# Kernel tuning notes

Measured on AMD Instinct MI355X. Metric: run time of the kernel, lower is better.

Reference implementation:

```python
import jax, jax.numpy as jnp
import numpy as np

DIM = 128
N_CONV = 4
N_GRAPHS = 256
EPS = 1e-5


def _layernorm(h, g, b):
    m = jnp.mean(h, axis=-1, keepdims=True)
    v = jnp.mean((h - m) ** 2, axis=-1, keepdims=True)
    return g * (h - m) / jnp.sqrt(v + 1e-5) + b


def _gated_gcn(x, ei, e, Wsrc, bsrc, Wdst, bdst, We, be, nxg, nxb, neg, neb):
    # x: [N, D] node feats, ei: [2, E], e: [E, D] edge feats
    n = x.shape[0]
    i, j = ei[0], ei[1]
    sig = jax.nn.sigmoid(e)                                   # [E, D]
    e_sum = jax.ops.segment_sum(sig, i, num_segments=n)       # [N, D]
    e_gated = sig / (e_sum[i] + EPS)                          # [E, D]
    msg = e_gated * (x[j] @ Wdst + bdst)                      # [E, D]
    agg = jax.ops.segment_sum(msg, i, num_segments=n)         # [N, D]
    out = x @ Wsrc + bsrc + agg
    out = x + jax.nn.silu(_layernorm(out, nxg, nxb))
    z = jnp.concatenate([x[i], x[j], e], axis=-1)             # [E, 3D]
    e_new = e + jax.nn.silu(_layernorm(z @ We + be, neg, neb))
    return out, e_new


def setup_inputs() -> dict:
    key = jax.random.key(0)
    ks = iter(jax.random.split(key, 64))
    d = DIM

    def rn(shape, s=0.05):
        return (jax.random.normal(next(ks), shape, dtype=jnp.float32) * s)

    inp = {}
    inp["x"] = jax.random.normal(next(ks), (20000, 92), dtype=jnp.float32)
    inp["edge_attr"] = jax.random.normal(next(ks), (320000, 50), dtype=jnp.float32)
    inp["edge_attr_line"] = jax.random.normal(next(ks), (600000, 40), dtype=jnp.float32)
    inp["edge_index"] = jax.random.randint(next(ks), (2, 320000), 0, 20000, dtype=jnp.int64)
    inp["edge_index_line"] = jax.random.randint(next(ks), (2, 600000), 0, 320000, dtype=jnp.int64)
    inp["batch"] = jnp.sort(jax.random.randint(next(ks), (20000,), 0, N_GRAPHS, dtype=jnp.int64))

    inp["pre1_W"] = rn((92, d)); inp["pre1_b"] = jnp.zeros((d,), jnp.float32)
    inp["pre2_W"] = rn((50, d)); inp["pre2_b"] = jnp.zeros((d,), jnp.float32)
    inp["pre3_W"] = rn((40, d)); inp["pre3_b"] = jnp.zeros((d,), jnp.float32)

    for pfx in ("line", "atom"):
        inp[pfx + "_Wsrc"] = rn((N_CONV, d, d)); inp[pfx + "_bsrc"] = jnp.zeros((N_CONV, d), jnp.float32)
        inp[pfx + "_Wdst"] = rn((N_CONV, d, d)); inp[pfx + "_bdst"] = jnp.zeros((N_CONV, d), jnp.float32)
        inp[pfx + "_We"] = rn((N_CONV, 3 * d, d)); inp[pfx + "_be"] = jnp.zeros((N_CONV, d), jnp.float32)
        inp[pfx + "_nxg"] = jnp.ones((N_CONV, d), jnp.float32); inp[pfx + "_nxb"] = jnp.zeros((N_CONV, d), jnp.float32)
        inp[pfx + "_neg"] = jnp.ones((N_CONV, d), jnp.float32); inp[pfx + "_neb"] = jnp.zeros((N_CONV, d), jnp.float32)

    inp["bn_g"] = jnp.ones((d,), jnp.float32); inp["bn_b"] = jnp.zeros((d,), jnp.float32)
    inp["post_W"] = rn((d, d)); inp["post_b"] = jnp.zeros((d,), jnp.float32)
    inp["out_W"] = rn((d, 1)); inp["out_b"] = jnp.zeros((1,), jnp.float32)
    return inp


def reference(x, edge_attr, edge_attr_line,
              pre1_W, pre1_b, pre2_W, pre2_b, pre3_W, pre3_b,
              line_Wsrc, line_bsrc, line_Wdst, line_bdst, line_We, line_be,
              line_nxg, line_nxb, line_neg, line_neb,
              atom_Wsrc, atom_bsrc, atom_Wdst, atom_bdst, atom_We, atom_be,
              atom_nxg, atom_nxb, atom_neg, atom_neb,
              bn_g, bn_b, post_W, post_b, out_W, out_b,
              edge_index, edge_index_line, batch):
    act = jax.nn.silu
    # pre-FC (single layer each)
    h_node = act(x @ pre1_W + pre1_b)              # [N, D]
    h_edge = act(edge_attr @ pre2_W + pre2_b)      # [E, D]
    h_line = act(edge_attr_line @ pre3_W + pre3_b) # [E_line, D]

    for l in range(N_CONV):
        # line graph conv: nodes = atom edges, edges = line-graph edges
        h_edge, h_line = _gated_gcn(h_edge, edge_index_line, h_line,
                                    line_Wsrc[l], line_bsrc[l], line_Wdst[l], line_bdst[l],
                                    line_We[l], line_be[l],
                                    line_nxg[l], line_nxb[l], line_neg[l], line_neb[l])
        # atom graph conv
        h_node, h_edge = _gated_gcn(h_node, edge_index, h_edge,
                                    atom_Wsrc[l], atom_bsrc[l], atom_Wdst[l], atom_bdst[l],
                                    atom_We[l], atom_be[l],
                                    atom_nxg[l], atom_nxb[l], atom_neg[l], atom_neb[l])
        # dropout_rate = 0 -> identity

    # BatchNorm1d (batch statistics over nodes)
    m = jnp.mean(h_node, axis=0)
    v = jnp.mean((h_node - m) ** 2, axis=0)
    out = bn_g * (h_node - m) / jnp.sqrt(v + 1e-5) + bn_b
    out = act(out)
    out = act(out @ post_W + post_b)

    # global mean pool over crystals
    sums = jax.ops.segment_sum(out, batch, num_segments=N_GRAPHS)
    cnts = jax.ops.segment_sum(jnp.ones((out.shape[0],), out.dtype), batch, num_segments=N_GRAPHS)
    pooled = sums / jnp.maximum(cnts, 1.0)[:, None]
    return (pooled @ out_W + out_b).reshape(-1)    # [N_GRAPHS]
```

## Files before the change

### kernel.cpp

```cpp
#include <hip/hip_runtime.h>

#define NCONV_DEF 4
#define SCH 1024

typedef unsigned short u16;
typedef __attribute__((ext_vector_type(8))) short s8v;
typedef __attribute__((ext_vector_type(4))) float f4v;
typedef __attribute__((ext_vector_type(8))) unsigned short u16x8;

__device__ __forceinline__ float sigm_f(float x){ return 1.f/(1.f+__expf(-x)); }
__device__ __forceinline__ float silu_f(float x){ return x/(1.f+__expf(-x)); }
__device__ __forceinline__ float b2f(u16 h){ union{unsigned u; float f;} v; v.u=(unsigned)h<<16; return v.f; }
__device__ __forceinline__ u16 f2b(float f){ union{float f; unsigned u;} v; v.f=f; unsigned r=v.u+0x7fffu+((v.u>>16)&1u); return (u16)(r>>16); }
__device__ __forceinline__ float ldAv(const float* p, size_t i){ return p[i]; }
__device__ __forceinline__ float ldAv(const u16* p, size_t i){ return b2f(p[i]); }

#define EPS_ 136

__global__ __launch_bounds__(256) void zero_f_k(float* p, long n){
    long i=(long)blockIdx.x*256+threadIdx.x, st=(long)gridDim.x*256;
    for(;i<n;i+=st) p[i]=0.f;
}
__global__ __launch_bounds__(256) void zero_i_k(int* p, long n){
    long i=(long)blockIdx.x*256+threadIdx.x, st=(long)gridDim.x*256;
    for(;i<n;i+=st) p[i]=0;
}
__global__ void diag_k(float* out, int n, float v){
    int i=blockIdx.x*256+threadIdx.x; if(i<n) out[i]=v;
}
__global__ void probe_k(const int* ei, const int* eil, const int* batch, int nb, int* flag){
    if(threadIdx.x||blockIdx.x) return;
    int a=2,b=2,c=2;
    for(int k=0;k<64;k++){ if(ei[2*k+1]!=0) a=1; if(eil[2*k+1]!=0) b=1; }
    int base=nb-128;
    for(int k=0;k<64;k++){ if(batch[base+2*k+1]!=0) c=1; }
    flag[0]=a; flag[1]=b; flag[2]=c;
}

__global__ __launch_bounds__(256)
void hist_k(const int* __restrict__ idx, const int* __restrict__ iflag, int fi,
            int* __restrict__ cnt, int Ne, int Nn){
    int e=blockIdx.x*256+threadIdx.x; if(e>=Ne) return;
    int st=iflag[fi];
    int i=idx[(size_t)e*st]; i=i<0?0:(i>=Nn?Nn-1:i);
    atomicAdd(&cnt[i],1);
}
__global__ __launch_bounds__(256)
void scan1_k(const int* cnt, int* tot, int n){
    __shared__ int sh[256];
    int base=blockIdx.x*SCH, s=0;
    for(int t=threadIdx.x;t<SCH;t+=256){ int i=base+t; s+=(i<n)?cnt[i]:0; }
    sh[threadIdx.x]=s; __syncthreads();
    for(int o=128;o;o>>=1){ if(threadIdx.x<o) sh[threadIdx.x]+=sh[threadIdx.x+o]; __syncthreads(); }
    if(threadIdx.x==0) tot[blockIdx.x]=sh[0];
}
__global__ void scan2_k(int* tot, int nb){
    if(threadIdx.x==0&&blockIdx.x==0){ int acc=0; for(int i=0;i<nb;i++){int v=tot[i]; tot[i]=acc; acc+=v;} }
}
__global__ __launch_bounds__(256)
void scan3_k(const int* cnt, const int* tot, int* off, int n, int total){
    __shared__ int sh[256];
    int b=blockIdx.x, t4=b*SCH+threadIdx.x*4;
    int v0=(t4+0<n)?cnt[t4+0]:0, v1=(t4+1<n)?cnt[t4+1]:0;
    int v2=(t4+2<n)?cnt[t4+2]:0, v3=(t4+3<n)?cnt[t4+3]:0;
    int ls=v0+v1+v2+v3;
    sh[threadIdx.x]=ls; __syncthreads();
    for(int o=1;o<256;o<<=1){
        int val=(threadIdx.x>=o)?sh[threadIdx.x-o]:0; __syncthreads();
        sh[threadIdx.x]+=val; __syncthreads();
    }
    int excl=sh[threadIdx.x]-ls+tot[b];
    if(t4+0<n) off[t4+0]=excl;
    if(t4+1<n) off[t4+1]=excl+v0;
    if(t4+2<n) off[t4+2]=excl+v0+v1;
    if(t4+3<n) off[t4+3]=excl+v0+v1+v2;
    if(b==(int)gridDim.x-1&&threadIdx.x==255) off[n]=total;
}
__global__ __launch_bounds__(256)
void fill_k(const int* __restrict__ idx, const int* __restrict__ iflag, int fi,
            const int* __restrict__ off, int* __restrict__ cur, int* __restrict__ list,
            int Ne, int Nn){
    int e=blockIdx.x*256+threadIdx.x; if(e>=Ne) return;
    int st=iflag[fi];
    int i=idx[(size_t)e*st]; i=i<0?0:(i>=Nn?Nn-1:i);
    int pos=off[i]+atomicAdd(&cur[i],1);
    list[pos]=e;
}

__global__ __launch_bounds__(256)
void pack_w_k(const float* __restrict__ W, u16* __restrict__ Wp, int K, int Kp){
    int i=blockIdx.x*256+threadIdx.x;
    if(i>=128*Kp) return;
    int n=i/Kp, k=i-n*Kp;
    Wp[i] = (k<K) ? f2b(W[(size_t)k*128+n]) : (u16)0;
}

template<typename TA, int ACT>
__global__ __launch_bounds__(256)
void gemm_k(const TA* __restrict__ A, int lda, int M, int K, int Kp,
            const u16* __restrict__ Wp, const float* __restrict__ bias,
            u16* __restrict__ C)
{
    __shared__ __align__(16) u16 As[64*72];
    __shared__ __align__(16) u16 Bs[128*72];
    const int tid=threadIdx.x, row0=blockIdx.x*64;
    const int w=tid>>6, l=tid&63, lr=l&15, kg=l>>4;
    f4v zz={0.f,0.f,0.f,0.f};
    f4v acc[8];
#pragma unroll
    for(int i=0;i<8;++i) acc[i]=zz;

    for(int kt=0;kt<Kp;kt+=64){
        {
            int r=tid>>2, c0=(tid&3)*16;
            int gr=row0+r;
            bool vec=false;
            if constexpr (sizeof(TA)==2) vec=((K&63)==0);
            if(vec){
                const u16* src=(const u16*)(const void*)A+(size_t)gr*lda+kt+c0;
                u16x8 v0={0,0,0,0,0,0,0,0}, v1={0,0,0,0,0,0,0,0};
                if(gr<M){ v0=*(const u16x8*)src; v1=*(const u16x8*)(src+8); }
                *(u16x8*)&As[r*72+c0]=v0;
                *(u16x8*)&As[r*72+c0+8]=v1;
            } else {
                for(int c=c0;c<c0+16;++c){
                    int k=kt+c;
                    float v=(gr<M&&k<K)?ldAv(A,(size_t)gr*lda+k):0.f;
                    As[r*72+c]=f2b(v);
                }
            }
        }
        {
            int n=tid>>1, k0=(tid&1)*32;
            const u16* src=Wp+(size_t)n*Kp+kt+k0;
            *(u16x8*)&Bs[n*72+k0]   =*(const u16x8*)(src);
            *(u16x8*)&Bs[n*72+k0+8] =*(const u16x8*)(src+8);
            *(u16x8*)&Bs[n*72+k0+16]=*(const u16x8*)(src+16);
            *(u16x8*)&Bs[n*72+k0+24]=*(const u16x8*)(src+24);
        }
        __syncthreads();
        const int arow=w*16+lr;
#pragma unroll
        for(int kk=0;kk<64;kk+=32){
            s8v a=*(const s8v*)&As[arow*72+kk+kg*8];
#pragma unroll
            for(int ct=0;ct<8;++ct){
                s8v bfr=*(const s8v*)&Bs[(ct*16+lr)*72+kk+kg*8];
                acc[ct]=__builtin_amdgcn_mfma_f32_16x16x32_bf16(a,bfr,acc[ct],0,0,0);
            }
        }
        __syncthreads();
    }
    u16* ep=Bs;
#pragma unroll
    for(int ct=0;ct<8;++ct){
        int col=ct*16+lr;
        float bv=bias?bias[col]:0.f;
#pragma unroll
        for(int reg=0;reg<4;++reg){
            float v=acc[ct][reg]+bv;
            if(ACT) v=silu_f(v);
            ep[(w*16+kg*4+reg)*EPS_+col]=f2b(v);
        }
    }
    __syncthreads();
    {
        int ar=tid>>2, gr=row0+ar;
        if(gr<M){
            u16* crow=C+(size_t)gr*128+(tid&3)*32;
            const u16* hrow=&ep[ar*EPS_+(tid&3)*32];
#pragma unroll
            for(int c4=0;c4<4;++c4)
                *(u16x8*)(crow+c4*8)=*(const u16x8*)(hrow+c4*8);
        }
    }
}

__global__ __launch_bounds__(256)
void gemmz_k(u16* __restrict__ X, int M,
             const u16* __restrict__ Wp, const float* __restrict__ bias,
             const u16* __restrict__ U,
             const float* __restrict__ g, const float* __restrict__ b)
{
    __shared__ __align__(16) u16 As[64*72];
    __shared__ __align__(16) u16 Bs[128*72];
    const int tid=threadIdx.x, row0=blockIdx.x*64;
    const int w=tid>>6, l=tid&63, lr=l&15, kg=l>>4;
    u16* ep=Bs;
    {
        int ar=tid>>2, gr=row0+ar;
        u16x8 z8={0,0,0,0,0,0,0,0};
        u16x8 u0=z8,u1=z8,u2=z8,u3=z8;
        if(gr<M){
            const u16* ur=U+(size_t)gr*128+(tid&3)*32;
            u0=*(const u16x8*)(ur); u1=*(const u16x8*)(ur+8);
            u2=*(const u16x8*)(ur+16); u3=*(const u16x8*)(ur+24);
        }
        u16* d=&ep[(tid>>2)*EPS_+(tid&3)*32];
        *(u16x8*)(d)=u0; *(u16x8*)(d+8)=u1; *(u16x8*)(d+16)=u2; *(u16x8*)(d+24)=u3;
    }
    __syncthreads();
    f4v acc[8];
#pragma unroll
    for(int ct=0;ct<8;++ct){
        int col=ct*16+lr;
        float bv=bias[col];
#pragma unroll
        for(int reg=0;reg<4;++reg)
            acc[ct][reg]=b2f(ep[(w*16+kg*4+reg)*EPS_+col])+bv;
    }
    __syncthreads();

    for(int kt=0;kt<128;kt+=64){
        {
            int r=tid>>2, c0=(tid&3)*16;
            int gr=row0+r;
            const u16* src=X+(size_t)gr*128+kt+c0;
            u16x8 v0={0,0,0,0,0,0,0,0}, v1={0,0,0,0,0,0,0,0};
            if(gr<M){ v0=*(const u16x8*)src; v1=*(const u16x8*)(src+8); }
            *(u16x8*)&As[r*72+c0]=v0;
            *(u16x8*)&As[r*72+c0+8]=v1;
        }
        {
            int n=tid>>1, k0=(tid&1)*32;
            const u16* src=Wp+(size_t)n*128+kt+k0;
            *(u16x8*)&Bs[n*72+k0]   =*(const u16x8*)(src);
            *(u16x8*)&Bs[n*72+k0+8] =*(const u16x8*)(src+8);
            *(u16x8*)&Bs[n*72+k0+16]=*(const u16x8*)(src+16);
            *(u16x8*)&Bs[n*72+k0+24]=*(const u16x8*)(src+24);
        }
        __syncthreads();
        const int arow=w*16+lr;
#pragma unroll
        for(int kk=0;kk<64;kk+=32){
            s8v a=*(const s8v*)&As[arow*72+kk+kg*8];
#pragma unroll
            for(int ct=0;ct<8;++ct){
                s8v bfr=*(const s8v*)&Bs[(ct*16+lr)*72+kk+kg*8];
                acc[ct]=__builtin_amdgcn_mfma_f32_16x16x32_bf16(a,bfr,acc[ct],0,0,0);
            }
        }
        __syncthreads();
    }
    float sum[4]={0.f,0.f,0.f,0.f}, sq[4]={0.f,0.f,0.f,0.f};
#pragma unroll
    for(int ct=0;ct<8;++ct)
#pragma unroll
        for(int reg=0;reg<4;++reg){
            float v=acc[ct][reg];
            sum[reg]+=v; sq[reg]+=v*v;
        }
#pragma unroll
    for(int m=1;m<16;m<<=1)
#pragma unroll
        for(int reg=0;reg<4;++reg){
            sum[reg]+=__shfl_xor(sum[reg],m,64);
            sq[reg] +=__shfl_xor(sq[reg], m,64);
        }
    float mean[4], rstd[4];
#pragma unroll
    for(int reg=0;reg<4;++reg){
        mean[reg]=sum[reg]*(1.f/128.f);
        float var=sq[reg]*(1.f/128.f)-mean[reg]*mean[reg];
        rstd[reg]=rsqrtf(var+1e-5f);
    }
#pragma unroll
    for(int ct=0;ct<8;++ct){
        int col=ct*16+lr;
        float gv=g[col], bv=b[col];
#pragma unroll
        for(int reg=0;reg<4;++reg){
            float h=gv*(acc[ct][reg]-mean[reg])*rstd[reg]+bv;
            ep[(w*16+kg*4+reg)*EPS_+col]=f2b(silu_f(h));
        }
    }
    __syncthreads();
    {
        int ar=tid>>2, gr=row0+ar;
        if(gr<M){
            u16* xrow=X+(size_t)gr*128+(tid&3)*32;
            const u16* hrow=&ep[ar*EPS_+(tid&3)*32];
#pragma unroll
            for(int c4=0;c4<4;++c4){
                u16x8 xv=*(const u16x8*)(xrow+c4*8);
                u16x8 hv=*(const u16x8*)(hrow+c4*8);
                u16x8 ov;
#pragma unroll
                for(int j=0;j<8;++j) ov[j]=f2b(b2f(xv[j])+b2f(hv[j]));
                *(u16x8*)(xrow+c4*8)=ov;
            }
        }
    }
}

template<int FIN, int HASPREV>
__global__ __launch_bounds__(256)
void gather_k(const u16* __restrict__ e, const u16* __restrict__ P1,
              u16* __restrict__ U,
              const int* __restrict__ off, const int* __restrict__ list,
              const int* __restrict__ idx, long joff,
              const int* __restrict__ iflag, int fi,
              int Nn, int c0, int c1)
{
    int st=iflag[fi];
    int wid=threadIdx.x>>6, lane=threadIdx.x&63;
    int n=blockIdx.x*4+wid; if(n>=Nn) return;
    int beg=off[n], end=off[n+1];
    float es0=0.f,es1=0.f,a0=0.f,a1=0.f;
    int k=beg;
    for(; k+1<end; k+=2){
        int eid0=list[k], eid1=list[k+1];
        int j0=idx[((size_t)joff+eid0)*st]; j0=j0<0?0:(j0>=Nn?Nn-1:j0);
        int j1=idx[((size_t)joff+eid1)*st]; j1=j1<0?0:(j1>=Nn?Nn-1:j1);
        bool in0=(j0>=c0)&&(j0<c1), in1=(j1>=c0)&&(j1<c1);
        if(FIN||in0){
            unsigned ev=*(const unsigned*)(e+(size_t)eid0*128+2*lane);
            float s0=sigm_f(b2f((u16)(ev&0xffff)));
            float s1=sigm_f(b2f((u16)(ev>>16)));
            if(FIN){ es0+=s0; es1+=s1; }
            if(in0){
                unsigned pv=*(const unsigned*)(P1+(size_t)(j0-c0)*128+2*lane);
                a0+=s0*b2f((u16)(pv&0xffff));
                a1+=s1*b2f((u16)(pv>>16));
            }
        }
        if(FIN||in1){
            unsigned ev=*(const unsigned*)(e+(size_t)eid1*128+2*lane);
            float s0=sigm_f(b2f((u16)(ev&0xffff)));
            float s1=sigm_f(b2f((u16)(ev>>16)));
            if(FIN){ es0+=s0; es1+=s1; }
            if(in1){
                unsigned pv=*(const unsigned*)(P1+(size_t)(j1-c0)*128+2*lane);
                a0+=s0*b2f((u16)(pv&0xffff));
                a1+=s1*b2f((u16)(pv>>16));
            }
        }
    }
    if(k<end){
        int eid=list[k];
        int j=idx[((size_t)joff+eid)*st]; j=j<0?0:(j>=Nn?Nn-1:j);
        bool in=(j>=c0)&&(j<c1);
        if(FIN||in){
            unsigned ev=*(const unsigned*)(e+(size_t)eid*128+2*lane);
            float s0=sigm_f(b2f((u16)(ev&0xffff)));
            float s1=sigm_f(b2f((u16)(ev>>16)));
            if(FIN){ es0+=s0; es1+=s1; }
            if(in){
                unsigned pv=*(const unsigned*)(P1+(size_t)(j-c0)*128+2*lane);
                a0+=s0*b2f((u16)(pv&0xffff));
                a1+=s1*b2f((u16)(pv>>16));
            }
        }
    }
    unsigned* up=(unsigned*)(U+(size_t)n*128+2*lane);
    if(!FIN){
        *up=((unsigned)f2b(a0))|((unsigned)f2b(a1)<<16);
    } else {
        if(HASPREV){
            unsigned pv=*up;
            a0+=b2f((u16)(pv&0xffff));
            a1+=b2f((u16)(pv>>16));
        }
        float r0=1.f/(es0+1e-5f), r1=1.f/(es1+1e-5f);
        *up=((unsigned)f2b(a0*r0))|((unsigned)f2b(a1*r1)<<16);
    }
}

__global__ __launch_bounds__(256)
void edgez_k(u16* __restrict__ e, const u16* __restrict__ x,
             const int* __restrict__ idx, long joff,
             const int* __restrict__ iflag, int fi,
             const u16* __restrict__ Wep, const float* __restrict__ be,
             const float* __restrict__ g, const float* __restrict__ b,
             int Ne, int Nn)
{
    __shared__ __align__(16) u16 As[64*72];
    __shared__ __align__(16) u16 Bs[128*72];
    __shared__ int rid[128];
    const int tid=threadIdx.x, row0=blockIdx.x*64;
    const int w=tid>>6, l=tid&63, lr=l&15, kg=l>>4;
    int st=iflag[fi];
    if(tid<128){
        int r=tid&63, eid=row0+r; if(eid>=Ne) eid=Ne-1;
        long elem=(tid<64)?(long)eid:(joff+eid);
        int v=idx[(size_t)elem*st]; v=v<0?0:(v>=Nn?Nn-1:v);
        rid[tid]=v;
    }
    __syncthreads();
    const int ar=tid>>2, ac=(tid&3)*16;
    const int bn=tid>>1, bk=(tid&1)*32;
    int eidA=row0+ar; if(eidA>=Ne) eidA=Ne-1;
    const u16* aptr0=x+(size_t)rid[ar]*128;
    const u16* aptr1=x+(size_t)rid[64+ar]*128;
    const u16* aptr2=e+(size_t)eidA*128;

    f4v zz={0.f,0.f,0.f,0.f};
    f4v acc[8];
#pragma unroll
    for(int i=0;i<8;++i) acc[i]=zz;

    u16x8 a0,a1,b0,b1,b2,b3;
    {
        const u16* src=aptr0+ac;
        a0=*(const u16x8*)src; a1=*(const u16x8*)(src+8);
        const u16* wsrc=Wep+(size_t)bn*384+bk;
        b0=*(const u16x8*)wsrc; b1=*(const u16x8*)(wsrc+8);
        b2=*(const u16x8*)(wsrc+16); b3=*(const u16x8*)(wsrc+24);
    }
    for(int s=0;s<6;++s){
        __syncthreads();
        *(u16x8*)&As[ar*72+ac]  =a0;
        *(u16x8*)&As[ar*72+ac+8]=a1;
        *(u16x8*)&Bs[bn*72+bk]   =b0;
        *(u16x8*)&Bs[bn*72+bk+8] =b1;
        *(u16x8*)&Bs[bn*72+bk+16]=b2;
        *(u16x8*)&Bs[bn*72+bk+24]=b3;
        if(s<5){
            int sn=s+1, sec=sn>>1, half=sn&1;
            const u16* src=(sec==0?aptr0:(sec==1?aptr1:aptr2))+half*64+ac;
            a0=*(const u16x8*)src; a1=*(const u16x8*)(src+8);
            const u16* wsrc=Wep+(size_t)bn*384+sn*64+bk;
            b0=*(const u16x8*)wsrc; b1=*(const u16x8*)(wsrc+8);
            b2=*(const u16x8*)(wsrc+16); b3=*(const u16x8*)(wsrc+24);
        }
        __syncthreads();
        __builtin_amdgcn_s_setprio(1);
        const int arow=w*16+lr;
#pragma unroll
        for(int kk=0;kk<64;kk+=32){
            s8v a=*(const s8v*)&As[arow*72+kk+kg*8];
#pragma unroll
            for(int ct=0;ct<8;++ct){
                s8v bfr=*(const s8v*)&Bs[(ct*16+lr)*72+kk+kg*8];
                acc[ct]=__builtin_amdgcn_mfma_f32_16x16x32_bf16(a,bfr,acc[ct],0,0,0);
            }
        }
        __builtin_amdgcn_s_setprio(0);
    }
    __syncthreads();
    float sum[4]={0.f,0.f,0.f,0.f}, sq[4]={0.f,0.f,0.f,0.f};
#pragma unroll
    for(int ct=0;ct<8;++ct){
        float bev=be[ct*16+lr];
#pragma unroll
        for(int reg=0;reg<4;++reg){
            float v=acc[ct][reg]+bev;
            acc[ct][reg]=v;
            sum[reg]+=v; sq[reg]+=v*v;
        }
    }
#pragma unroll
    for(int m=1;m<16;m<<=1){
#pragma unroll
        for(int reg=0;reg<4;++reg){
            sum[reg]+=__shfl_xor(sum[reg],m,64);
            sq[reg] +=__shfl_xor(sq[reg], m,64);
        }
    }
    float mean[4], rstd[4];
#pragma unroll
    for(int reg=0;reg<4;++reg){
        mean[reg]=sum[reg]*(1.f/128.f);
        float var=sq[reg]*(1.f/128.f)-mean[reg]*mean[reg];
        rstd[reg]=rsqrtf(var+1e-5f);
    }
    u16* ep=Bs;
#pragma unroll
    for(int ct=0;ct<8;++ct){
        int col=ct*16+lr;
        float gv=g[col], bv=b[col];
#pragma unroll
        for(int reg=0;reg<4;++reg){
            float h=gv*(acc[ct][reg]-mean[reg])*rstd[reg]+bv;
            ep[(w*16+kg*4+reg)*EPS_+col]=f2b(silu_f(h));
        }
    }
    __syncthreads();
    {
        int eid=row0+ar;
        if(eid<Ne){
            u16* erow=e+(size_t)eid*128+(tid&3)*32;
            const u16* hrow=&ep[ar*EPS_+(tid&3)*32];
#pragma unroll
            for(int c4=0;c4<4;++c4){
                u16x8 ev=*(const u16x8*)(erow+c4*8);
                u16x8 hv=*(const u16x8*)(hrow+c4*8);
                u16x8 ov;
#pragma unroll
                for(int j=0;j<8;++j) ov[j]=f2b(b2f(ev[j])+b2f(hv[j]));
                *(u16x8*)(erow+c4*8)=ov;
            }
        }
    }
}

__global__ __launch_bounds__(256)
void bn_stats_k(const u16* __restrict__ h, float* __restrict__ st, int N){
    int t=blockIdx.x*256+threadIdx.x;
    int d=t&127, r0=t>>7, rstride=(gridDim.x*256)>>7;
    float s=0.f,q=0.f;
    for(int r=r0;r<N;r+=rstride){ float v=b2f(h[(size_t)r*128+d]); s+=v; q+=v*v; }
    atomicAdd(&st[d],s); atomicAdd(&st[128+d],q);
}
__global__ __launch_bounds__(256)
void bn_apply_k(u16* __restrict__ h, const float* __restrict__ st,
                const float* __restrict__ g, const float* __restrict__ b, int N){
    int t=blockIdx.x*256+threadIdx.x;
    if(t>=N*128) return;
    int d=t&127;
    float inv=1.f/(float)N;
    float m=st[d]*inv, var=st[128+d]*inv-m*m;
    float v=g[d]*(b2f(h[t])-m)*rsqrtf(var+1e-5f)+b[d];
    h[t]=f2b(silu_f(v));
}
__global__ __launch_bounds__(256)
void pool_k(const u16* __restrict__ o, const int* __restrict__ batch,
            const int* __restrict__ iflag,
            float* __restrict__ pooled, float* __restrict__ cnt, int N, int NG){
    int st=iflag[2];
    int wid=threadIdx.x>>6, lane=threadIdx.x&63;
    int n=blockIdx.x*4+wid; if(n>=N) return;
    int gi=batch[(size_t)n*st]; gi=gi<0?0:(gi>=NG?NG-1:gi);
    atomicAdd(&pooled[(size_t)gi*128+lane],    b2f(o[(size_t)n*128+lane]));
    atomicAdd(&pooled[(size_t)gi*128+64+lane], b2f(o[(size_t)n*128+64+lane]));
    if(lane==0) atomicAdd(&cnt[gi],1.f);
}
__global__ void final_k(const float* __restrict__ pooled, const float* __restrict__ cnt,
                        const float* __restrict__ oW, const float* __restrict__ ob,
                        float* __restrict__ out){
    int gi=blockIdx.x, lane=threadIdx.x;
    float v=pooled[(size_t)gi*128+lane]*oW[lane]
           +pooled[(size_t)gi*128+64+lane]*oW[64+lane];
    for(int m=32;m;m>>=1) v+=__shfl_xor(v,m,64);
    if(lane==0) out[gi]=v/fmaxf(cnt[gi],1.f)+ob[0];
}

template<typename TA>
static inline void gemm(hipStream_t s, const TA* A, int lda, int M, int K, int Kp,
                        const u16* Wp, const float* bias, u16* C, int act){
    dim3 grid((M+63)/64);
    if(act) gemm_k<TA,1><<<grid,256,0,s>>>(A,lda,M,K,Kp,Wp,bias,C);
    else    gemm_k<TA,0><<<grid,256,0,s>>>(A,lda,M,K,Kp,Wp,bias,C);
}

static inline void build_csr(hipStream_t s, const int* idx, int fi, const int* iflag,
                             int Ne, int Nn, int* off, int* cur, int* list, int* tot){
    int nb=(Nn+SCH-1)/SCH;
    zero_i_k<<<256,256,0,s>>>(cur,Nn);
    hist_k<<<(Ne+255)/256,256,0,s>>>(idx,iflag,fi,cur,Ne,Nn);
    scan1_k<<<nb,256,0,s>>>(cur,tot,Nn);
    scan2_k<<<1,1,0,s>>>(tot,nb);
    scan3_k<<<nb,256,0,s>>>(cur,tot,off,Nn,Ne);
    zero_i_k<<<256,256,0,s>>>(cur,Nn);
    fill_k<<<(Ne+255)/256,256,0,s>>>(idx,iflag,fi,off,cur,list,Ne,Nn);
}

static inline void pack_w(hipStream_t s, const float* W, u16* Wp, int K, int Kp){
    pack_w_k<<<(128*Kp+255)/256,256,0,s>>>(W,Wp,K,Kp);
}

extern "C" void kernel_launch(void* const* d_in, const int* in_sizes, int n_in,
                              void* d_out, int out_size, void* d_ws, size_t ws_size,
                              hipStream_t stream)
{
    const float* x_in =(const float*)d_in[0];
    const float* ea   =(const float*)d_in[1];
    const float* eal  =(const float*)d_in[2];
    const int*   ei   =(const int*)d_in[3];
    const int*   eil  =(const int*)d_in[4];
    const int*   batch=(const int*)d_in[5];
    const float* pre1W=(const float*)d_in[6];  const float* pre1b=(const float*)d_in[7];
    const float* pre2W=(const float*)d_in[8];  const float* pre2b=(const float*)d_in[9];
    const float* pre3W=(const float*)d_in[10]; const float* pre3b=(const float*)d_in[11];
    const float* lWsrc=(const float*)d_in[12]; const float* lbsrc=(const float*)d_in[13];
    const float* lWdst=(const float*)d_in[14]; const float* lbdst=(const float*)d_in[15];
    const float* lWe  =(const float*)d_in[16]; const float* lbe  =(const float*)d_in[17];
    const float* lnxg =(const float*)d_in[18]; const float* lnxb =(const float*)d_in[19];
    const float* lneg =(const float*)d_in[20]; const float* lneb =(const float*)d_in[21];
    const float* aWsrc=(const float*)d_in[22]; const float* absrc=(const float*)d_in[23];
    const float* aWdst=(const float*)d_in[24]; const float* abdst=(const float*)d_in[25];
    const float* aWe  =(const float*)d_in[26]; const float* abe  =(const float*)d_in[27];
    const float* anxg =(const float*)d_in[28]; const float* anxb =(const float*)d_in[29];
    const float* aneg =(const float*)d_in[30]; const float* aneb =(const float*)d_in[31];
    const float* bng  =(const float*)d_in[32]; const float* bnb  =(const float*)d_in[33];
    const float* postW=(const float*)d_in[34]; const float* postb=(const float*)d_in[35];
    const float* outW =(const float*)d_in[36]; const float* outb =(const float*)d_in[37];
    (void)n_in;

    const int N =in_sizes[5];
    const int E =in_sizes[3]/2;
    const int EL=in_sizes[4]/2;
    const int NG=out_size;
    const int CH=(E+1)/2;

    char* base=(char*)d_ws;
    size_t off=0;
    auto alloc=[&](size_t bytes)->char*{
        char* p=base+off; off=(off+bytes+255)&~(size_t)255; return p;
    };
    u16* hN   =(u16*)alloc((size_t)N*128*2);
    u16* hE   =(u16*)alloc((size_t)E*128*2);
    u16* hL   =(u16*)alloc((size_t)EL*128*2);
    u16* U    =(u16*)alloc((size_t)E*128*2);
    u16* P1   =(u16*)alloc((size_t)CH*128*2);
    int* off_l=(int*)alloc((size_t)(E+1)*4);
    int* cur_l=(int*)alloc((size_t)E*4);
    int* list_l=(int*)alloc((size_t)EL*4);
    int* off_a=(int*)alloc((size_t)(N+1)*4);
    int* cur_a=(int*)alloc((size_t)N*4);
    int* list_a=(int*)alloc((size_t)E*4);
    int* tot  =(int*)alloc(4096);
    int* iflag=(int*)alloc(64);
    float* stats =(float*)alloc(256*4);
    float* pooled=(float*)alloc((size_t)NG*128*4);
    float* cnt   =(float*)alloc((size_t)NG*4);
    u16* pre1p=(u16*)alloc(128*128*2);
    u16* pre2p=(u16*)alloc(128*64*2);
    u16* pre3p=(u16*)alloc(128*64*2);
    u16* postp=(u16*)alloc(128*128*2);
    u16 *lsrcp[4],*ldstp[4],*lWep[4],*asrcp[4],*adstp[4],*aWep[4];
    for(int i=0;i<4;i++){
        lsrcp[i]=(u16*)alloc(128*128*2);
        ldstp[i]=(u16*)alloc(128*128*2);
        lWep[i] =(u16*)alloc(128*384*2);
        asrcp[i]=(u16*)alloc(128*128*2);
        adstp[i]=(u16*)alloc(128*128*2);
        aWep[i] =(u16*)alloc(128*384*2);
    }
    if(off>ws_size){
        diag_k<<<(NG+255)/256,256,0,stream>>>((float*)d_out,NG,(float)(ws_size>>20)+0.25f);
        return;
    }

    probe_k<<<1,64,0,stream>>>(ei,eil,batch,N,iflag);
    build_csr(stream,eil,1,iflag,EL,E,off_l,cur_l,list_l,tot);
    build_csr(stream,ei, 0,iflag,E, N,off_a,cur_a,list_a,tot);

    pack_w(stream,pre1W,pre1p,92,128);
    pack_w(stream,pre2W,pre2p,50,64);
    pack_w(stream,pre3W,pre3p,40,64);
    pack_w(stream,postW,postp,128,128);
    for(int i=0;i<4;i++){
        pack_w(stream,lWsrc+(size_t)i*128*128,lsrcp[i],128,128);
        pack_w(stream,lWdst+(size_t)i*128*128,ldstp[i],128,128);
        pack_w(stream,lWe  +(size_t)i*384*128,lWep[i],384,384);
        pack_w(stream,aWsrc+(size_t)i*128*128,asrcp[i],128,128);
        pack_w(stream,aWdst+(size_t)i*128*128,adstp[i],128,128);
        pack_w(stream,aWe  +(size_t)i*384*128,aWep[i],384,384);
    }

    gemm(stream,x_in,92,N, 92,128,pre1p,pre1b,hN,1);
    gemm(stream,ea,  50,E, 50, 64,pre2p,pre2b,hE,1);
    gemm(stream,eal, 40,EL,40, 64,pre3p,pre3b,hL,1);

    for(int l=0;l<NCONV_DEF;++l){
        {
            gemm(stream,hE,128,CH,128,128,ldstp[l],lbdst+l*128,P1,0);
            gather_k<0,0><<<(E+3)/4,256,0,stream>>>(hL,P1,U,off_l,list_l,
                                                    eil,EL,iflag,1,E,0,CH);
            gemm(stream,hE+(size_t)CH*128,128,E-CH,128,128,ldstp[l],lbdst+l*128,P1,0);
            gather_k<1,1><<<(E+3)/4,256,0,stream>>>(hL,P1,U,off_l,list_l,
                                                    eil,EL,iflag,1,E,CH,E);
            edgez_k<<<(EL+63)/64,256,0,stream>>>(hL,hE,eil,EL,iflag,1,
                                                 lWep[l],lbe+l*128,lneg+l*128,lneb+l*128,EL,E);
            gemmz_k<<<(E+63)/64,256,0,stream>>>(hE,E,lsrcp[l],lbsrc+l*128,U,
                                                lnxg+l*128,lnxb+l*128);
        }
        {
            gemm(stream,hN,128,N,128,128,adstp[l],abdst+l*128,P1,0);
            gather_k<1,0><<<(N+3)/4,256,0,stream>>>(hE,P1,U,off_a,list_a,
                                                    ei,E,iflag,0,N,0,N);
            edgez_k<<<(E+63)/64,256,0,stream>>>(hE,hN,ei,E,iflag,0,
                                                aWep[l],abe+l*128,aneg+l*128,aneb+l*128,E,N);
            gemmz_k<<<(N+63)/64,256,0,stream>>>(hN,N,asrcp[l],absrc+l*128,U,
                                                anxg+l*128,anxb+l*128);
        }
    }

    zero_f_k<<<64,256,0,stream>>>(stats,256);
    zero_f_k<<<64,256,0,stream>>>(pooled,(long)NG*128);
    zero_f_k<<<1,256,0,stream>>>(cnt,NG);
    bn_stats_k<<<256,256,0,stream>>>(hN,stats,N);
    bn_apply_k<<<(N*128+255)/256,256,0,stream>>>(hN,stats,bng,bnb,N);

    gemm(stream,hN,128,N,128,128,postp,postb,P1,1);

    pool_k<<<(N+3)/4,256,0,stream>>>(P1,batch,iflag,pooled,cnt,N,NG);
    final_k<<<NG,64,0,stream>>>(pooled,cnt,outW,outb,(float*)d_out);
}
```

Baseline: 3.640 ms.

## Precompute neighbor ids in CSR, double-buffer edge GEMM LDS, reuse loaded edge rows

The CSR fill now stores each edge's source-neighbor index in a parallel jlist. This removes the dependent strided index lookup from every gather iteration across all 4 layers. edgez_k double-buffers its shared-memory tiles to drop per-stage barriers, and keeps the edge-feature slice already loaded for the GEMM in registers for the residual add instead of re-reading global memory. gemmz_k loads the full K=128 tile in one pass with a single barrier. The cost is extra LDS use per block and an extra int array per graph, and the barrier removals need careful buffer aliasing to stay race-free.

```diff
diff --git a/kernel.cpp b/kernel.cpp
--- a/kernel.cpp
+++ b/kernel.cpp
@@ -77,14 +77,15 @@
     if(b==(int)gridDim.x-1&&threadIdx.x==255) off[n]=total;
 }
 __global__ __launch_bounds__(256)
-void fill_k(const int* __restrict__ idx, const int* __restrict__ iflag, int fi,
-            const int* __restrict__ off, int* __restrict__ cur, int* __restrict__ list,
-            int Ne, int Nn){
+void fill_k(const int* __restrict__ idx, const int* __restrict__ iflag, int fi, long joff,
+            const int* __restrict__ off, int* __restrict__ cur,
+            int* __restrict__ list, int* __restrict__ jlist, int Ne, int Nn){
     int e=blockIdx.x*256+threadIdx.x; if(e>=Ne) return;
     int st=iflag[fi];
     int i=idx[(size_t)e*st]; i=i<0?0:(i>=Nn?Nn-1:i);
+    int j=idx[((size_t)joff+e)*st]; j=j<0?0:(j>=Nn?Nn-1:j);
     int pos=off[i]+atomicAdd(&cur[i],1);
-    list[pos]=e;
+    list[pos]=e; jlist[pos]=j;
 }
 
 __global__ __launch_bounds__(256)
@@ -182,13 +183,13 @@
              const u16* __restrict__ U,
              const float* __restrict__ g, const float* __restrict__ b)
 {
-    __shared__ __align__(16) u16 As[64*72];
-    __shared__ __align__(16) u16 Bs[128*72];
+    __shared__ __align__(16) u16 As[2][64*68];
+    __shared__ __align__(16) u16 Bs[128*136];
     const int tid=threadIdx.x, row0=blockIdx.x*64;
     const int w=tid>>6, l=tid&63, lr=l&15, kg=l>>4;
-    u16* ep=Bs;
+    u16* ep=&As[0][0];
+    const int ar=tid>>2, gr=row0+ar;
     {
-        int ar=tid>>2, gr=row0+ar;
         u16x8 z8={0,0,0,0,0,0,0,0};
         u16x8 u0=z8,u1=z8,u2=z8,u3=z8;
         if(gr<M){
@@ -196,7 +197,7 @@
             u0=*(const u16x8*)(ur); u1=*(const u16x8*)(ur+8);
             u2=*(const u16x8*)(ur+16); u3=*(const u16x8*)(ur+24);
         }
-        u16* d=&ep[(tid>>2)*EPS_+(tid&3)*32];
+        u16* d=&ep[ar*EPS_+(tid&3)*32];
         *(u16x8*)(d)=u0; *(u16x8*)(d+8)=u1; *(u16x8*)(d+16)=u2; *(u16x8*)(d+24)=u3;
     }
     __syncthreads();
@@ -211,36 +212,36 @@
     }
     __syncthreads();
 
-    for(int kt=0;kt<128;kt+=64){
-        {
-            int r=tid>>2, c0=(tid&3)*16;
-            int gr=row0+r;
-            const u16* src=X+(size_t)gr*128+kt+c0;
-            u16x8 v0={0,0,0,0,0,0,0,0}, v1={0,0,0,0,0,0,0,0};
-            if(gr<M){ v0=*(const u16x8*)src; v1=*(const u16x8*)(src+8); }
-            *(u16x8*)&As[r*72+c0]=v0;
-            *(u16x8*)&As[r*72+c0+8]=v1;
-        }
-        {
-            int n=tid>>1, k0=(tid&1)*32;
-            const u16* src=Wp+(size_t)n*128+kt+k0;
-            *(u16x8*)&Bs[n*72+k0]   =*(const u16x8*)(src);
-            *(u16x8*)&Bs[n*72+k0+8] =*(const u16x8*)(src+8);
-            *(u16x8*)&Bs[n*72+k0+16]=*(const u16x8*)(src+16);
-            *(u16x8*)&Bs[n*72+k0+24]=*(const u16x8*)(src+24);
-        }
-        __syncthreads();
-        const int arow=w*16+lr;
+    {
+        int c0=(tid&3)*16;
+        const u16* src=X+(size_t)gr*128;
+        u16x8 z8={0,0,0,0,0,0,0,0};
+        u16x8 v0=z8,v1=z8,v2=z8,v3=z8;
+        if(gr<M){
+            v0=*(const u16x8*)(src+c0);    v1=*(const u16x8*)(src+c0+8);
+            v2=*(const u16x8*)(src+64+c0); v3=*(const u16x8*)(src+64+c0+8);
+        }
+        *(u16x8*)&As[0][ar*68+c0]=v0;  *(u16x8*)&As[0][ar*68+c0+8]=v1;
+        *(u16x8*)&As[1][ar*68+c0]=v2;  *(u16x8*)&As[1][ar*68+c0+8]=v3;
+        int bn=tid>>1, bk=(tid&1)*64;
+        const u16* wsrc=Wp+(size_t)bn*128+bk;
+#pragma unroll
+        for(int q=0;q<8;++q)
+            *(u16x8*)&Bs[bn*136+bk+q*8]=*(const u16x8*)(wsrc+q*8);
+    }
+    __syncthreads();
+    const int arow=w*16+lr;
+#pragma unroll
+    for(int kt=0;kt<2;++kt){
 #pragma unroll
         for(int kk=0;kk<64;kk+=32){
-            s8v a=*(const s8v*)&As[arow*72+kk+kg*8];
+            s8v a=*(const s8v*)&As[kt][arow*68+kk+kg*8];
 #pragma unroll
             for(int ct=0;ct<8;++ct){
-                s8v bfr=*(const s8v*)&Bs[(ct*16+lr)*72+kk+kg*8];
+                s8v bfr=*(const s8v*)&Bs[(ct*16+lr)*136+kt*64+kk+kg*8];
                 acc[ct]=__builtin_amdgcn_mfma_f32_16x16x32_bf16(a,bfr,acc[ct],0,0,0);
             }
         }
-        __syncthreads();
     }
     float sum[4]={0.f,0.f,0.f,0.f}, sq[4]={0.f,0.f,0.f,0.f};
 #pragma unroll
@@ -264,6 +265,7 @@
         float var=sq[reg]*(1.f/128.f)-mean[reg]*mean[reg];
         rstd[reg]=rsqrtf(var+1e-5f);
     }
+    __syncthreads();
 #pragma unroll
     for(int ct=0;ct<8;++ct){
         int col=ct*16+lr;
@@ -274,21 +276,17 @@
             ep[(w*16+kg*4+reg)*EPS_+col]=f2b(silu_f(h));
         }
     }
-    __syncthreads();
-    {
-        int ar=tid>>2, gr=row0+ar;
-        if(gr<M){
-            u16* xrow=X+(size_t)gr*128+(tid&3)*32;
-            const u16* hrow=&ep[ar*EPS_+(tid&3)*32];
-#pragma unroll
-            for(int c4=0;c4<4;++c4){
-                u16x8 xv=*(const u16x8*)(xrow+c4*8);
-                u16x8 hv=*(const u16x8*)(hrow+c4*8);
-                u16x8 ov;
-#pragma unroll
-                for(int j=0;j<8;++j) ov[j]=f2b(b2f(xv[j])+b2f(hv[j]));
-                *(u16x8*)(xrow+c4*8)=ov;
-            }
+    if(gr<M){
+        u16* xrow=X+(size_t)gr*128+(tid&3)*32;
+        const u16* hrow=&ep[ar*EPS_+(tid&3)*32];
+#pragma unroll
+        for(int c4=0;c4<4;++c4){
+            u16x8 xv=*(const u16x8*)(xrow+c4*8);
+            u16x8 hv=*(const u16x8*)(hrow+c4*8);
+            u16x8 ov;
+#pragma unroll
+            for(int j=0;j<8;++j) ov[j]=f2b(b2f(xv[j])+b2f(hv[j]));
+            *(u16x8*)(xrow+c4*8)=ov;
         }
     }
 }
@@ -298,47 +296,15 @@
 void gather_k(const u16* __restrict__ e, const u16* __restrict__ P1,
               u16* __restrict__ U,
               const int* __restrict__ off, const int* __restrict__ list,
-              const int* __restrict__ idx, long joff,
-              const int* __restrict__ iflag, int fi,
+              const int* __restrict__ jlist,
               int Nn, int c0, int c1)
 {
-    int st=iflag[fi];
     int wid=threadIdx.x>>6, lane=threadIdx.x&63;
     int n=blockIdx.x*4+wid; if(n>=Nn) return;
     int beg=off[n], end=off[n+1];
     float es0=0.f,es1=0.f,a0=0.f,a1=0.f;
-    int k=beg;
-    for(; k+1<end; k+=2){
-        int eid0=list[k], eid1=list[k+1];
-        int j0=idx[((size_t)joff+eid0)*st]; j0=j0<0?0:(j0>=Nn?Nn-1:j0);
-        int j1=idx[((size_t)joff+eid1)*st]; j1=j1<0?0:(j1>=Nn?Nn-1:j1);
-        bool in0=(j0>=c0)&&(j0<c1), in1=(j1>=c0)&&(j1<c1);
-        if(FIN||in0){
-            unsigned ev=*(const unsigned*)(e+(size_t)eid0*128+2*lane);
-            float s0=sigm_f(b2f((u16)(ev&0xffff)));
-            float s1=sigm_f(b2f((u16)(ev>>16)));
-            if(FIN){ es0+=s0; es1+=s1; }
-            if(in0){
-                unsigned pv=*(const unsigned*)(P1+(size_t)(j0-c0)*128+2*lane);
-                a0+=s0*b2f((u16)(pv&0xffff));
-                a1+=s1*b2f((u16)(pv>>16));
-            }
-        }
-        if(FIN||in1){
-            unsigned ev=*(const unsigned*)(e+(size_t)eid1*128+2*lane);
-            float s0=sigm_f(b2f((u16)(ev&0xffff)));
-            float s1=sigm_f(b2f((u16)(ev>>16)));
-            if(FIN){ es0+=s0; es1+=s1; }
-            if(in1){
-                unsigned pv=*(const unsigned*)(P1+(size_t)(j1-c0)*128+2*lane);
-                a0+=s0*b2f((u16)(pv&0xffff));
-                a1+=s1*b2f((u16)(pv>>16));
-            }
-        }
-    }
-    if(k<end){
-        int eid=list[k];
-        int j=idx[((size_t)joff+eid)*st]; j=j<0?0:(j>=Nn?Nn-1:j);
+    for(int k=beg;k<end;++k){
+        int eid=list[k], j=jlist[k];
         bool in=(j>=c0)&&(j<c1);
         if(FIN||in){
             unsigned ev=*(const unsigned*)(e+(size_t)eid*128+2*lane);
@@ -374,8 +340,8 @@
              const float* __restrict__ g, const float* __restrict__ b,
              int Ne, int Nn)
 {
-    __shared__ __align__(16) u16 As[64*72];
-    __shared__ __align__(16) u16 Bs[128*72];
+    __shared__ __align__(16) u16 As[2][64*68];
+    __shared__ __align__(16) u16 Bs[2][128*68];
     __shared__ int rid[128];
     const int tid=threadIdx.x, row0=blockIdx.x*64;
     const int w=tid>>6, l=tid&63, lr=l&15, kg=l>>4;
@@ -400,6 +366,7 @@
     for(int i=0;i<8;++i) acc[i]=zz;
 
     u16x8 a0,a1,b0,b1,b2,b3;
+    u16x8 er0,er1,er2,er3;
     {
         const u16* src=aptr0+ac;
         a0=*(const u16x8*)src; a1=*(const u16x8*)(src+8);
@@ -407,18 +374,20 @@
         b0=*(const u16x8*)wsrc; b1=*(const u16x8*)(wsrc+8);
         b2=*(const u16x8*)(wsrc+16); b3=*(const u16x8*)(wsrc+24);
     }
+#pragma unroll
     for(int s=0;s<6;++s){
-        __syncthreads();
-        *(u16x8*)&As[ar*72+ac]  =a0;
-        *(u16x8*)&As[ar*72+ac+8]=a1;
-        *(u16x8*)&Bs[bn*72+bk]   =b0;
-        *(u16x8*)&Bs[bn*72+bk+8] =b1;
-        *(u16x8*)&Bs[bn*72+bk+16]=b2;
-        *(u16x8*)&Bs[bn*72+bk+24]=b3;
+        const int buf=s&1;
+        *(u16x8*)&As[buf][ar*68+ac]  =a0;
+        *(u16x8*)&As[buf][ar*68+ac+8]=a1;
+        *(u16x8*)&Bs[buf][bn*68+bk]   =b0;
+        *(u16x8*)&Bs[buf][bn*68+bk+8] =b1;
+        *(u16x8*)&Bs[buf][bn*68+bk+16]=b2;
+        *(u16x8*)&Bs[buf][bn*68+bk+24]=b3;
         if(s<5){
-            int sn=s+1, sec=sn>>1, half=sn&1;
+            const int sn=s+1, sec=sn>>1, half=sn&1;
             const u16* src=(sec==0?aptr0:(sec==1?aptr1:aptr2))+half*64+ac;
             a0=*(const u16x8*)src; a1=*(const u16x8*)(src+8);
+            if(sec==2){ if(half==0){ er0=a0; er1=a1; } else { er2=a0; er3=a1; } }
             const u16* wsrc=Wep+(size_t)bn*384+sn*64+bk;
             b0=*(const u16x8*)wsrc; b1=*(const u16x8*)(wsrc+8);
             b2=*(const u16x8*)(wsrc+16); b3=*(const u16x8*)(wsrc+24);
@@ -428,16 +397,15 @@
         const int arow=w*16+lr;
 #pragma unroll
         for(int kk=0;kk<64;kk+=32){
-            s8v a=*(const s8v*)&As[arow*72+kk+kg*8];
+            s8v a=*(const s8v*)&As[buf][arow*68+kk+kg*8];
 #pragma unroll
             for(int ct=0;ct<8;++ct){
-                s8v bfr=*(const s8v*)&Bs[(ct*16+lr)*72+kk+kg*8];
+                s8v bfr=*(const s8v*)&Bs[buf][(ct*16+lr)*68+kk+kg*8];
                 acc[ct]=__builtin_amdgcn_mfma_f32_16x16x32_bf16(a,bfr,acc[ct],0,0,0);
             }
         }
         __builtin_amdgcn_s_setprio(0);
     }
-    __syncthreads();
     float sum[4]={0.f,0.f,0.f,0.f}, sq[4]={0.f,0.f,0.f,0.f};
 #pragma unroll
     for(int ct=0;ct<8;++ct){
@@ -464,7 +432,7 @@
         float var=sq[reg]*(1.f/128.f)-mean[reg]*mean[reg];
         rstd[reg]=rsqrtf(var+1e-5f);
     }
-    u16* ep=Bs;
+    u16* ep=&Bs[0][0];
 #pragma unroll
     for(int ct=0;ct<8;++ct){
         int col=ct*16+lr;
@@ -475,21 +443,23 @@
             ep[(w*16+kg*4+reg)*EPS_+col]=f2b(silu_f(h));
         }
     }
-    __syncthreads();
     {
         int eid=row0+ar;
         if(eid<Ne){
-            u16* erow=e+(size_t)eid*128+(tid&3)*32;
-            const u16* hrow=&ep[ar*EPS_+(tid&3)*32];
-#pragma unroll
-            for(int c4=0;c4<4;++c4){
-                u16x8 ev=*(const u16x8*)(erow+c4*8);
-                u16x8 hv=*(const u16x8*)(hrow+c4*8);
-                u16x8 ov;
-#pragma unroll
-                for(int j=0;j<8;++j) ov[j]=f2b(b2f(ev[j])+b2f(hv[j]));
-                *(u16x8*)(erow+c4*8)=ov;
+            u16* erow=e+(size_t)eid*128;
+            const u16* hr=&ep[ar*EPS_];
+            u16x8 h0=*(const u16x8*)(hr+ac),    h1=*(const u16x8*)(hr+ac+8);
+            u16x8 h2=*(const u16x8*)(hr+64+ac), h3=*(const u16x8*)(hr+64+ac+8);
+            u16x8 o0,o1,o2,o3;
+#pragma unroll
+            for(int j=0;j<8;++j){
+                o0[j]=f2b(b2f(er0[j])+b2f(h0[j]));
+                o1[j]=f2b(b2f(er1[j])+b2f(h1[j]));
+                o2[j]=f2b(b2f(er2[j])+b2f(h2[j]));
+                o3[j]=f2b(b2f(er3[j])+b2f(h3[j]));
             }
+            *(u16x8*)(erow+ac)=o0;    *(u16x8*)(erow+ac+8)=o1;
+            *(u16x8*)(erow+64+ac)=o2; *(u16x8*)(erow+64+ac+8)=o3;
         }
     }
 }
@@ -543,8 +513,8 @@
     else    gemm_k<TA,0><<<grid,256,0,s>>>(A,lda,M,K,Kp,Wp,bias,C);
 }
 
-static inline void build_csr(hipStream_t s, const int* idx, int fi, const int* iflag,
-                             int Ne, int Nn, int* off, int* cur, int* list, int* tot){
+static inline void build_csr(hipStream_t s, const int* idx, int fi, long joff, const int* iflag,
+                             int Ne, int Nn, int* off, int* cur, int* list, int* jlist, int* tot){
     int nb=(Nn+SCH-1)/SCH;
     zero_i_k<<<256,256,0,s>>>(cur,Nn);
     hist_k<<<(Ne+255)/256,256,0,s>>>(idx,iflag,fi,cur,Ne,Nn);
@@ -552,7 +522,7 @@
     scan2_k<<<1,1,0,s>>>(tot,nb);
     scan3_k<<<nb,256,0,s>>>(cur,tot,off,Nn,Ne);
     zero_i_k<<<256,256,0,s>>>(cur,Nn);
-    fill_k<<<(Ne+255)/256,256,0,s>>>(idx,iflag,fi,off,cur,list,Ne,Nn);
+    fill_k<<<(Ne+255)/256,256,0,s>>>(idx,iflag,fi,joff,off,cur,list,jlist,Ne,Nn);
 }
 
 static inline void pack_w(hipStream_t s, const float* W, u16* Wp, int K, int Kp){
@@ -606,9 +576,11 @@
     int* off_l=(int*)alloc((size_t)(E+1)*4);
     int* cur_l=(int*)alloc((size_t)E*4);
     int* list_l=(int*)alloc((size_t)EL*4);
+    int* jlist_l=(int*)alloc((size_t)EL*4);
     int* off_a=(int*)alloc((size_t)(N+1)*4);
     int* cur_a=(int*)alloc((size_t)N*4);
     int* list_a=(int*)alloc((size_t)E*4);
+    int* jlist_a=(int*)alloc((size_t)E*4);
     int* tot  =(int*)alloc(4096);
     int* iflag=(int*)alloc(64);
     float* stats =(float*)alloc(256*4);
@@ -633,8 +605,8 @@
     }
 
     probe_k<<<1,64,0,stream>>>(ei,eil,batch,N,iflag);
-    build_csr(stream,eil,1,iflag,EL,E,off_l,cur_l,list_l,tot);
-    build_csr(stream,ei, 0,iflag,E, N,off_a,cur_a,list_a,tot);
+    build_csr(stream,eil,1,EL,iflag,EL,E,off_l,cur_l,list_l,jlist_l,tot);
+    build_csr(stream,ei, 0,E, iflag,E, N,off_a,cur_a,list_a,jlist_a,tot);
 
     pack_w(stream,pre1W,pre1p,92,128);
     pack_w(stream,pre2W,pre2p,50,64);
@@ -656,11 +628,9 @@
     for(int l=0;l<NCONV_DEF;++l){
         {
             gemm(stream,hE,128,CH,128,128,ldstp[l],lbdst+l*128,P1,0);
-            gather_k<0,0><<<(E+3)/4,256,0,stream>>>(hL,P1,U,off_l,list_l,
-                                                    eil,EL,iflag,1,E,0,CH);
+            gather_k<0,0><<<(E+3)/4,256,0,stream>>>(hL,P1,U,off_l,list_l,jlist_l,E,0,CH);
             gemm(stream,hE+(size_t)CH*128,128,E-CH,128,128,ldstp[l],lbdst+l*128,P1,0);
-            gather_k<1,1><<<(E+3)/4,256,0,stream>>>(hL,P1,U,off_l,list_l,
-                                                    eil,EL,iflag,1,E,CH,E);
+            gather_k<1,1><<<(E+3)/4,256,0,stream>>>(hL,P1,U,off_l,list_l,jlist_l,E,CH,E);
             edgez_k<<<(EL+63)/64,256,0,stream>>>(hL,hE,eil,EL,iflag,1,
                                                  lWep[l],lbe+l*128,lneg+l*128,lneb+l*128,EL,E);
             gemmz_k<<<(E+63)/64,256,0,stream>>>(hE,E,lsrcp[l],lbsrc+l*128,U,
@@ -668,8 +638,7 @@
         }
         {
             gemm(stream,hN,128,N,128,128,adstp[l],abdst+l*128,P1,0);
-            gather_k<1,0><<<(N+3)/4,256,0,stream>>>(hE,P1,U,off_a,list_a,
-                                                    ei,E,iflag,0,N,0,N);
+            gather_k<1,0><<<(N+3)/4,256,0,stream>>>(hE,P1,U,off_a,list_a,jlist_a,N,0,N);
             edgez_k<<<(E+63)/64,256,0,stream>>>(hE,hN,ei,E,iflag,0,
                                                 aWep[l],abe+l*128,aneg+l*128,aneb+l*128,E,N);
             gemmz_k<<<(N+63)/64,256,0,stream>>>(hN,N,asrcp[l],absrc+l*128,U,
```

Measured after the change: 3.663 ms. Within noise of the previous version (+0.7%).
